# Optimization experiments

Hardware: AMD Instinct MI355X
Metric: run time of the kernel (lower is better)

## Reference

```python
import jax, jax.numpy as jnp
import numpy as np

B, S, D = 2, 2048, 2048
NH, NKV, HD = 16, 4, 128
ROPE_BASE = 10000.0
NEG = -1e9


def _rope_tables(seq_len, dim):
    inv_freq = 1.0 / ROPE_BASE ** (jnp.arange(0, dim, 2, dtype=jnp.float32) / dim)
    t = jnp.arange(seq_len, dtype=jnp.float32)
    freqs = jnp.outer(t, inv_freq)                      # [S, dim/2]
    return jnp.cos(freqs), jnp.sin(freqs)


def _apply_rope(x, cos, sin):
    # x: [B, S, H, HD]; interleaved-pair rotation matching the original module
    x1 = x[..., ::2]
    x2 = x[..., 1::2]
    c = cos[None, :, None, :]
    s = sin[None, :, None, :]
    out1 = x1 * c - x2 * s
    out2 = x1 * s + x2 * c
    return jnp.stack([out1, out2], axis=-1).reshape(x.shape)


def setup_inputs() -> dict:
    key = jax.random.key(0)
    ks = jax.random.split(key, 5)
    x = jax.random.normal(ks[0], (B, S, D), dtype=jnp.float32)
    # causal additive mask [1, 1, S, S]
    causal = jnp.tril(jnp.ones((S, S), dtype=jnp.bool_))
    mask = jnp.where(causal, 0.0, NEG).astype(jnp.float32)[None, None]
    Wq = jax.random.normal(ks[1], (D, NH * HD), dtype=jnp.float32) * (D ** -0.5)
    Wk = jax.random.normal(ks[2], (D, NKV * HD), dtype=jnp.float32) * (D ** -0.5)
    Wv = jax.random.normal(ks[3], (D, NKV * HD), dtype=jnp.float32) * (D ** -0.5)
    Wo = jax.random.normal(ks[4], (NH * HD, D), dtype=jnp.float32) * ((NH * HD) ** -0.5)
    return {"x": x, "mask": mask, "Wq": Wq, "Wk": Wk, "Wv": Wv, "Wo": Wo}


def reference(x, mask, Wq, Wk, Wv, Wo):
    b, s, _ = x.shape
    q = (x @ Wq).reshape(b, s, NH, HD)
    k = (x @ Wk).reshape(b, s, NKV, HD)
    v = (x @ Wv).reshape(b, s, NKV, HD)

    cos, sin = _rope_tables(s, HD)
    q = _apply_rope(q, cos, sin)
    k = _apply_rope(k, cos, sin)

    rep = NH // NKV
    k = jnp.repeat(k, rep, axis=2)                       # [b, s, NH, HD]
    v = jnp.repeat(v, rep, axis=2)

    q = q.transpose(0, 2, 1, 3)                          # [b, NH, s, HD]
    k = k.transpose(0, 2, 1, 3)
    v = v.transpose(0, 2, 1, 3)

    scores = jnp.einsum('bhqd,bhkd->bhqk', q, k) / jnp.sqrt(jnp.float32(HD))
    scores = scores + mask
    attn = jax.nn.softmax(scores, axis=-1)
    out = jnp.einsum('bhqk,bhkd->bhqd', attn, v)
    out = out.transpose(0, 2, 1, 3).reshape(b, s, NH * HD)
    return out @ Wo
```

## Files before the change

kernel.cpp:

```cpp
#include <hip/hip_runtime.h>
#include <stdint.h>

#define B_    2
#define S_    2048
#define D_    2048
#define NH_   16
#define NKV_  4
#define HD_   128
#define M_    (B_*S_)
#define NQKV_ 3072

typedef __bf16 bf16x8 __attribute__((ext_vector_type(8)));
typedef float  f32x4  __attribute__((ext_vector_type(4)));

__device__ __forceinline__ unsigned short f2bf(float f) {
    unsigned int u = __float_as_uint(f);
    u += 0x7fffu + ((u >> 16) & 1u);
    return (unsigned short)(u >> 16);
}

__device__ __forceinline__ unsigned short cvt_bf(float f) {
    __bf16 b = (__bf16)f;
    return *(unsigned short*)&b;
}

__device__ __forceinline__ void async_cp16(const unsigned short* g, unsigned short* l) {
    __builtin_amdgcn_global_load_lds((const __attribute__((address_space(1))) void*)g,
                                     (__attribute__((address_space(3))) void*)l, 16, 0, 0);
}

__global__ void prep(const float* __restrict__ x, unsigned short* __restrict__ xb,
                     const float* __restrict__ Wq, const float* __restrict__ Wk,
                     const float* __restrict__ Wv, const float* __restrict__ Wo,
                     unsigned short* __restrict__ Wqkvt, unsigned short* __restrict__ Wot,
                     float2* __restrict__ ctab) {
    __shared__ float tile[32][33];
    const int blk = blockIdx.x, tid = threadIdx.x;

    if (blk < 8192) {
        int idx = blk * 256 + tid;
        float4 v = ((const float4*)x)[idx];
        unsigned int lo = (unsigned int)f2bf(v.x) | ((unsigned int)f2bf(v.y) << 16);
        unsigned int hi = (unsigned int)f2bf(v.z) | ((unsigned int)f2bf(v.w) << 16);
        ((uint2*)xb)[idx] = make_uint2(lo, hi);
    } else if (blk < 18432) {
        const float* src; unsigned short* dst; int ncols, nx, bxy;
        if (blk < 12288)      { src = Wq; dst = Wqkvt;             ncols = 2048; nx = 64; bxy = blk - 8192; }
        else if (blk < 13312) { src = Wk; dst = Wqkvt + 2048*2048; ncols = 512;  nx = 16; bxy = blk - 12288; }
        else if (blk < 14336) { src = Wv; dst = Wqkvt + 2560*2048; ncols = 512;  nx = 16; bxy = blk - 13312; }
        else                  { src = Wo; dst = Wot;               ncols = 2048; nx = 64; bxy = blk - 14336; }
        int n0 = (bxy & (nx - 1)) * 32, k0 = (bxy / nx) * 32;
        int tx = tid & 31, ty = tid >> 5;
#pragma unroll
        for (int i = 0; i < 4; i++) {
            int k = k0 + ty + i * 8;
            tile[ty + i * 8][tx] = src[(long)k * ncols + n0 + tx];
        }
        __syncthreads();
#pragma unroll
        for (int i = 0; i < 4; i++) {
            int n = n0 + ty + i * 8;
            dst[(long)n * 2048 + k0 + tx] = f2bf(tile[tx][ty + i * 8]);
        }
    } else {
        int gid = (blk - 18432) * 256 + tid;
        int s = gid >> 6, i = gid & 63;
        float inv = exp2f(-(float)i * 0.20762050593046014f);
        float ang = (float)s * inv;
        float sn, cs; sincosf(ang, &sn, &cs);
        ctab[gid] = make_float2(cs, sn);
    }
}


__device__ __forceinline__ bf16x8 lds_frag(const unsigned short* hb, int r, int ks, int quad) {
    int p = (r * 128 + ks * 64 + quad * 16) ^ ((r & 4) << 3);
    return *(const bf16x8*)((const char*)hb + p);
}

__device__ __forceinline__ void stage_half(const unsigned short* g, int Kel,
                                           unsigned short* lhalf, int wid, int lane) {
#pragma unroll
    for (int i = 0; i < 2; i++) {
        int chunk = wid * 2 + i;
        int o = chunk * 1024 + lane * 16;
        int row = o >> 7;
        int cb = (o & 127) ^ ((row & 4) << 3);
        async_cp16((const unsigned short*)((const char*)g + (size_t)row * Kel * 2 + cb),
                   lhalf + chunk * 512);
    }
}

template<int MB, int NB>
__device__ __forceinline__ void cluster(f32x4 (*acc)[4], bf16x8 (*a)[2], bf16x8 (*b)[2]) {
    __builtin_amdgcn_sched_barrier(0);
    __builtin_amdgcn_s_barrier();
    asm volatile("s_waitcnt lgkmcnt(0)" ::: "memory");
    __builtin_amdgcn_sched_barrier(0);
    __builtin_amdgcn_s_setprio(1);
#pragma unroll
    for (int ks = 0; ks < 2; ks++)
#pragma unroll
        for (int mi = 0; mi < 4; mi++)
#pragma unroll
            for (int ni = 0; ni < 2; ni++)
                acc[MB + mi][NB + ni] = __builtin_amdgcn_mfma_f32_16x16x32_bf16(
                    a[mi][ks], b[ni][ks], acc[MB + mi][NB + ni], 0, 0, 0);
    __builtin_amdgcn_s_setprio(0);
    __builtin_amdgcn_sched_barrier(0);
    __builtin_amdgcn_s_barrier();
    __builtin_amdgcn_sched_barrier(0);
}

__device__ __forceinline__ void gemm256_core(const unsigned short* __restrict__ A,
                                             const unsigned short* __restrict__ Bt,
                                             const int K, const int m0, const int n0,
                                             char* sm, f32x4 (*acc)[4]) {
    const int tid  = threadIdx.x;
    const int lane = tid & 63, wid = tid >> 6;
    const int quad = lane >> 4, l16 = lane & 15;
    const int wm = wid >> 2, wn = wid & 3;

    unsigned short* sA00 = (unsigned short*)(sm);
    unsigned short* sA01 = (unsigned short*)(sm + 16384);
    unsigned short* sA10 = (unsigned short*)(sm + 32768);
    unsigned short* sA11 = (unsigned short*)(sm + 49152);
    unsigned short* sB00 = (unsigned short*)(sm + 65536);
    unsigned short* sB01 = (unsigned short*)(sm + 81920);
    unsigned short* sB10 = (unsigned short*)(sm + 98304);
    unsigned short* sB11 = (unsigned short*)(sm + 114688);

    const unsigned short* A0 = A  + (size_t)m0 * K;
    const unsigned short* A1 = A  + (size_t)(m0 + 128) * K;
    const unsigned short* B0 = Bt + (size_t)n0 * K;
    const unsigned short* B1 = Bt + (size_t)(n0 + 128) * K;

    stage_half(A0,      K, sA00, wid, lane);
    stage_half(B1,      K, sB01, wid, lane);
    stage_half(A1,      K, sA01, wid, lane);
    stage_half(B0,      K, sB00, wid, lane);
    __builtin_amdgcn_sched_barrier(0);
    stage_half(A0 + 64, K, sA10, wid, lane);
    stage_half(B1 + 64, K, sB11, wid, lane);
    stage_half(A1 + 64, K, sA11, wid, lane);
    asm volatile("s_waitcnt vmcnt(6)" ::: "memory");
    __builtin_amdgcn_sched_barrier(0);
    __builtin_amdgcn_s_barrier();
    __builtin_amdgcn_sched_barrier(0);

    const int NIT = K >> 7;
    for (int j = 0; j < NIT; ++j) {
        const bool st = (j < NIT - 1);
        const int kof1 = (2 * j + 1) * 64;
        const int kof2 = (2 * j + 2) * 64;
        const int kof3 = (2 * j + 3) * 64;
        bf16x8 af[4][2], bA[2][2], bB[2][2];

#pragma unroll
        for (int mi = 0; mi < 4; mi++)
#pragma unroll
            for (int ks = 0; ks < 2; ks++)
                af[mi][ks] = lds_frag(sA00, wm * 64 + mi * 16 + l16, ks, quad);
#pragma unroll
        for (int ni = 0; ni < 2; ni++)
#pragma unroll
            for (int ks = 0; ks < 2; ks++)
                bA[ni][ks] = lds_frag(sB00, wn * 32 + ni * 16 + l16, ks, quad);
        stage_half(B0 + kof1, K, sB10, wid, lane);
        cluster<0, 0>(acc, af, bA);

#pragma unroll
        for (int ni = 0; ni < 2; ni++)
#pragma unroll
            for (int ks = 0; ks < 2; ks++)
                bB[ni][ks] = lds_frag(sB01, wn * 32 + ni * 16 + l16, ks, quad);
        if (st) stage_half(A0 + kof2, K, sA00, wid, lane);
        cluster<0, 2>(acc, af, bB);

#pragma unroll
        for (int mi = 0; mi < 4; mi++)
#pragma unroll
            for (int ks = 0; ks < 2; ks++)
                af[mi][ks] = lds_frag(sA01, wm * 64 + mi * 16 + l16, ks, quad);
        if (st) stage_half(B1 + kof2, K, sB01, wid, lane);
        cluster<4, 2>(acc, af, bB);

#pragma unroll
        for (int ni = 0; ni < 2; ni++)
#pragma unroll
            for (int ks = 0; ks < 2; ks++)
                bA[ni][ks] = lds_frag(sB00, wn * 32 + ni * 16 + l16, ks, quad);
        if (st) {
            stage_half(A1 + kof2, K, sA01, wid, lane);
            asm volatile("s_waitcnt vmcnt(6)" ::: "memory");
        } else {
            asm volatile("s_waitcnt vmcnt(0)" ::: "memory");
        }
        cluster<4, 0>(acc, af, bA);

#pragma unroll
        for (int mi = 0; mi < 4; mi++)
#pragma unroll
            for (int ks = 0; ks < 2; ks++)
                af[mi][ks] = lds_frag(sA10, wm * 64 + mi * 16 + l16, ks, quad);
#pragma unroll
        for (int ni = 0; ni < 2; ni++)
#pragma unroll
            for (int ks = 0; ks < 2; ks++)
                bA[ni][ks] = lds_frag(sB10, wn * 32 + ni * 16 + l16, ks, quad);
        if (st) stage_half(B0 + kof2, K, sB00, wid, lane);
        cluster<0, 0>(acc, af, bA);

#pragma unroll
        for (int ni = 0; ni < 2; ni++)
#pragma unroll
            for (int ks = 0; ks < 2; ks++)
                bB[ni][ks] = lds_frag(sB11, wn * 32 + ni * 16 + l16, ks, quad);
        if (st) stage_half(A0 + kof3, K, sA10, wid, lane);
        cluster<0, 2>(acc, af, bB);

#pragma unroll
        for (int mi = 0; mi < 4; mi++)
#pragma unroll
            for (int ks = 0; ks < 2; ks++)
                af[mi][ks] = lds_frag(sA11, wm * 64 + mi * 16 + l16, ks, quad);
        if (st) stage_half(B1 + kof3, K, sB11, wid, lane);
        cluster<4, 2>(acc, af, bB);

#pragma unroll
        for (int ni = 0; ni < 2; ni++)
#pragma unroll
            for (int ks = 0; ks < 2; ks++)
                bA[ni][ks] = lds_frag(sB10, wn * 32 + ni * 16 + l16, ks, quad);
        if (st) {
            stage_half(A1 + kof3, K, sA11, wid, lane);
            asm volatile("s_waitcnt vmcnt(6)" ::: "memory");
        }
        cluster<4, 0>(acc, af, bA);
    }
}

__global__ __launch_bounds__(512, 2) void gemm_qkv256(const unsigned short* __restrict__ A,
                                                      const unsigned short* __restrict__ Bt,
                                                      const float2* __restrict__ ctab,
                                                      unsigned short* __restrict__ Qr,
                                                      unsigned short* __restrict__ Kr,
                                                      unsigned short* __restrict__ Vt) {
    extern __shared__ char sm[];
    const int m0 = blockIdx.y * 256, n0 = blockIdx.x * 256;
    f32x4 acc[8][4] = {};
    gemm256_core(A, Bt, D_, m0, n0, sm, acc);

    const int tid  = threadIdx.x;
    const int lane = tid & 63, wid = tid >> 6;
    const int quad = lane >> 4, l16 = lane & 15;
    const int wm = wid >> 2, wn = wid & 3;

    if (n0 < 2048) {
#pragma unroll
        for (int mt = 0; mt < 8; mt++) {
            int rowb = m0 + ((mt & 4) << 5) + wm * 64 + (mt & 3) * 16 + quad * 4;
#pragma unroll
            for (int nt = 0; nt < 4; nt++) {
                int col = n0 + ((nt & 2) << 6) + wn * 32 + (nt & 1) * 16 + l16;
                int h = col >> 7, d = col & 127;
#pragma unroll
                for (int r = 0; r < 4; r++) {
                    int row = rowb + r;
                    int s = row & 2047, b = row >> 11;
                    float2 cs = ctab[s * 64 + (d >> 1)];
                    float own = acc[mt][nt][r];
                    float other = __shfl_xor(own, 1);
                    float val = (d & 1) ? (other * cs.y + own * cs.x)
                                        : (own * cs.x - other * cs.y);
                    Qr[((size_t)(b * 16 + h) * 2048 + s) * 128 + d] = f2bf(val);
                }
            }
        }
    } else if (n0 < 2560) {
#pragma unroll
        for (int mt = 0; mt < 8; mt++) {
            int rowb = m0 + ((mt & 4) << 5) + wm * 64 + (mt & 3) * 16 + quad * 4;
#pragma unroll
            for (int nt = 0; nt < 4; nt++) {
                int col = n0 + ((nt & 2) << 6) + wn * 32 + (nt & 1) * 16 + l16;
                int kvh = (col - 2048) >> 7, d = col & 127;
#pragma unroll
                for (int r = 0; r < 4; r++) {
                    int row = rowb + r;
                    int s = row & 2047, b = row >> 11;
                    float2 cs = ctab[s * 64 + (d >> 1)];
                    float own = acc[mt][nt][r];
                    float other = __shfl_xor(own, 1);
                    float val = (d & 1) ? (other * cs.y + own * cs.x)
                                        : (own * cs.x - other * cs.y);
                    Kr[((size_t)(b * 4 + kvh) * 2048 + s) * 128 + d] = f2bf(val);
                }
            }
        }
    } else {
        unsigned short* tr = (unsigned short*)sm;
#pragma unroll
        for (int mt = 0; mt < 8; mt++) {
            int slb = ((mt & 4) << 5) + wm * 64 + (mt & 3) * 16 + quad * 4;
#pragma unroll
            for (int nt = 0; nt < 4; nt++) {
                int cl = ((nt & 2) << 6) + wn * 32 + (nt & 1) * 16 + l16;
#pragma unroll
                for (int r = 0; r < 4; r++)
                    tr[cl * 256 + ((slb + r) ^ ((cl & 7) << 3))] = f2bf(acc[mt][nt][r]);
            }
        }
        __syncthreads();
        const int bb = m0 >> 11, sbase = m0 & 2047;
#pragma unroll
        for (int pass = 0; pass < 16; pass++) {
            int idx = pass * 512 + tid;
            int cl = idx >> 5, sch = idx & 31;
            uint4 v = *(const uint4*)&tr[cl * 256 + ((sch * 8) ^ ((cl & 7) << 3))];
            int col = n0 + cl;
            int kvh = (col - 2560) >> 7, d = col & 127;
            *(uint4*)&Vt[((size_t)(bb * 4 + kvh) * 128 + d) * 2048 + sbase + sch * 8] = v;
        }
    }
}

__global__ __launch_bounds__(512, 2) void gemm_bt128x256(const unsigned short* __restrict__ A,
                                                         const unsigned short* __restrict__ Bt,
                                                         float* __restrict__ C) {
    extern __shared__ char sm[];
    const int K = NH_ * HD_;
    const int tid  = threadIdx.x;
    const int lane = tid & 63, wid = tid >> 6;
    const int quad = lane >> 4, l16 = lane & 15;
    const int wm = wid >> 2, wn = wid & 3;
    const int m0 = blockIdx.y * 128, n0 = blockIdx.x * 256;

    unsigned short* sA0  = (unsigned short*)(sm);
    unsigned short* sA1  = (unsigned short*)(sm + 16384);
    unsigned short* sB00 = (unsigned short*)(sm + 32768);
    unsigned short* sB01 = (unsigned short*)(sm + 49152);
    unsigned short* sB10 = (unsigned short*)(sm + 65536);
    unsigned short* sB11 = (unsigned short*)(sm + 81920);

    const unsigned short* A0 = A  + (size_t)m0 * K;
    const unsigned short* B0 = Bt + (size_t)n0 * K;
    const unsigned short* B1 = Bt + (size_t)(n0 + 128) * K;

    f32x4 acc[4][4] = {};

    stage_half(A0,      K, sA0,  wid, lane);
    stage_half(B0,      K, sB00, wid, lane);
    stage_half(B1,      K, sB01, wid, lane);
    __builtin_amdgcn_sched_barrier(0);
    stage_half(A0 + 64, K, sA1,  wid, lane);
    stage_half(B0 + 64, K, sB10, wid, lane);
    asm volatile("s_waitcnt vmcnt(6)" ::: "memory");
    __builtin_amdgcn_sched_barrier(0);
    __builtin_amdgcn_s_barrier();
    __builtin_amdgcn_sched_barrier(0);

    const int NIT = K >> 7;
    for (int j = 0; j < NIT; ++j) {
        const bool st = (j < NIT - 1);
        const int t1 = (2 * j + 1) * 64;
        const int t2 = (2 * j + 2) * 64;
        const int t3 = (2 * j + 3) * 64;
        bf16x8 af[4][2], bb[2][2];

#pragma unroll
        for (int mi = 0; mi < 4; mi++)
#pragma unroll
            for (int ks = 0; ks < 2; ks++)
                af[mi][ks] = lds_frag(sA0, wm * 64 + mi * 16 + l16, ks, quad);
#pragma unroll
        for (int ni = 0; ni < 2; ni++)
#pragma unroll
            for (int ks = 0; ks < 2; ks++)
                bb[ni][ks] = lds_frag(sB00, wn * 32 + ni * 16 + l16, ks, quad);
        stage_half(B1 + t1, K, sB11, wid, lane);
        asm volatile("s_waitcnt vmcnt(6)" ::: "memory");
        cluster<0, 0>(acc, af, bb);

#pragma unroll
        for (int ni = 0; ni < 2; ni++)
#pragma unroll
            for (int ks = 0; ks < 2; ks++)
                bb[ni][ks] = lds_frag(sB01, wn * 32 + ni * 16 + l16, ks, quad);
        if (st) {
            stage_half(A0 + t2, K, sA0,  wid, lane);
            stage_half(B0 + t2, K, sB00, wid, lane);
            asm volatile("s_waitcnt vmcnt(6)" ::: "memory");
        } else {
            asm volatile("s_waitcnt vmcnt(2)" ::: "memory");
        }
        cluster<0, 2>(acc, af, bb);

#pragma unroll
        for (int mi = 0; mi < 4; mi++)
#pragma unroll
            for (int ks = 0; ks < 2; ks++)
                af[mi][ks] = lds_frag(sA1, wm * 64 + mi * 16 + l16, ks, quad);
#pragma unroll
        for (int ni = 0; ni < 2; ni++)
#pragma unroll
            for (int ks = 0; ks < 2; ks++)
                bb[ni][ks] = lds_frag(sB10, wn * 32 + ni * 16 + l16, ks, quad);
        if (st) {
            stage_half(B1 + t2, K, sB01, wid, lane);
            asm volatile("s_waitcnt vmcnt(6)" ::: "memory");
        } else {
            asm volatile("s_waitcnt vmcnt(0)" ::: "memory");
        }
        cluster<0, 0>(acc, af, bb);

#pragma unroll
        for (int ni = 0; ni < 2; ni++)
#pragma unroll
            for (int ks = 0; ks < 2; ks++)
                bb[ni][ks] = lds_frag(sB11, wn * 32 + ni * 16 + l16, ks, quad);
        if (st) {
            stage_half(A0 + t3, K, sA1,  wid, lane);
            stage_half(B0 + t3, K, sB10, wid, lane);
            asm volatile("s_waitcnt vmcnt(6)" ::: "memory");
        }
        cluster<0, 2>(acc, af, bb);
    }

#pragma unroll
    for (int mi = 0; mi < 4; mi++) {
        int rowb = m0 + wm * 64 + mi * 16 + quad * 4;
#pragma unroll
        for (int nb = 0; nb < 2; nb++)
#pragma unroll
            for (int ni = 0; ni < 2; ni++) {
                int col = n0 + nb * 128 + wn * 32 + ni * 16 + l16;
#pragma unroll
                for (int r = 0; r < 4; r++)
                    C[(size_t)(rowb + r) * 2048 + col] = acc[mi][nb * 2 + ni][r];
            }
    }
}

__global__ __launch_bounds__(256) void attn_fwd(const unsigned short* __restrict__ Qr,
                                                const unsigned short* __restrict__ Kr,
                                                const unsigned short* __restrict__ Vt,
                                                unsigned short* __restrict__ O) {
    __shared__ char KsB[64 * 256];
    __shared__ char VsB[128 * 128];
    __shared__ unsigned short Ps[4][16][72];
    const int tid  = threadIdx.x;
    const int lane = tid & 63, wid = tid >> 6;
    const int quad = lane >> 4, l16 = lane & 15;
    const int pid = blockIdx.x, h = blockIdx.y, b = blockIdx.z;
    const int kvh = h >> 2;
    const unsigned short* qp = Qr + (long)(b * NH_ + h) * S_ * HD_;
    const char* kpB = (const char*)(Kr + (long)(b * NKV_ + kvh) * S_ * HD_);
    const char* vpB = (const char*)(Vt + (long)(b * NKV_ + kvh) * HD_ * S_);
    const float sc2 = 0.08838834764831845f * 1.4426950408889634f;

    const int wKb = (tid * 16) ^ ((((tid >> 4) & 7)) << 4);
    const int wVb = (tid * 16) ^ ((((tid >> 3) & 7)) << 4);
    const int gKb = tid * 16;
    const int gVb = (tid >> 3) * (S_ * 2) + (tid & 7) * 16;
    int kro[4], vro[2];
#pragma unroll
    for (int ks = 0; ks < 4; ks++)
        kro[ks] = l16 * 256 + ((ks * 64 + quad * 16) ^ ((l16 & 7) << 4));
#pragma unroll
    for (int ks2 = 0; ks2 < 2; ks2++)
        vro[ks2] = l16 * 128 + ((ks2 * 64 + quad * 16) ^ ((l16 & 7) << 4));

    bf16x8 ones;
#pragma unroll
    for (int i = 0; i < 8; i++) ones[i] = (__bf16)1.0f;

    for (int phase = 0; phase < 2; phase++) {
        const int qt = phase ? pid : 31 - pid;
        const int qw = qt * 64 + wid * 16;

        bf16x8 aq[4];
#pragma unroll
        for (int ks = 0; ks < 4; ks++)
            aq[ks] = *(const bf16x8*)&qp[(long)(qw + l16) * HD_ + ks * 32 + quad * 8];

        f32x4 o[8] = {};
        float mi[4], li[4];
#pragma unroll
        for (int r = 0; r < 4; r++) { mi[r] = -3.0e38f; li[r] = 0.f; }

        for (int kt = 0; kt <= qt; kt++) {
            const int kv0 = kt * 64;
            const char* kg = kpB + (size_t)kv0 * 256 + gKb;
            const char* vg = vpB + (size_t)kv0 * 2 + gVb;
            __syncthreads();
#pragma unroll
            for (int i = 0; i < 4; i++)
                *(uint4*)(KsB + wKb + i * 4096) = *(const uint4*)(kg + i * 4096);
#pragma unroll
            for (int i = 0; i < 4; i++)
                *(uint4*)(VsB + wVb + i * 4096) = *(const uint4*)(vg + (size_t)i * 32 * (S_ * 2));
            __syncthreads();

            f32x4 s[4] = {};
#pragma unroll
            for (int ks = 0; ks < 4; ks++)
#pragma unroll
                for (int nt = 0; nt < 4; nt++) {
                    bf16x8 kb = *(const bf16x8*)&KsB[kro[ks] + nt * 4096];
                    s[nt] = __builtin_amdgcn_mfma_f32_16x16x32_bf16(aq[ks], kb, s[nt], 0, 0, 0);
                }

            float mt4[4];
#pragma unroll
            for (int r = 0; r < 4; r++) mt4[r] = -3.0e38f;
            if (kv0 + 63 > qw) {
#pragma unroll
                for (int nt = 0; nt < 4; nt++) {
                    int kvp = kv0 + nt * 16 + l16;
#pragma unroll
                    for (int r = 0; r < 4; r++) {
                        float sv = s[nt][r] * sc2;
                        sv = (kvp <= qw + quad * 4 + r) ? sv : -1.0e30f;
                        s[nt][r] = sv;
                        mt4[r] = fmaxf(mt4[r], sv);
                    }
                }
            } else {
#pragma unroll
                for (int nt = 0; nt < 4; nt++)
#pragma unroll
                    for (int r = 0; r < 4; r++) {
                        float sv = s[nt][r] * sc2;
                        s[nt][r] = sv;
                        mt4[r] = fmaxf(mt4[r], sv);
                    }
            }
#pragma unroll
            for (int off = 1; off < 16; off <<= 1)
#pragma unroll
                for (int r = 0; r < 4; r++)
                    mt4[r] = fmaxf(mt4[r], __shfl_xor(mt4[r], off));

            bool grew = false;
#pragma unroll
            for (int r = 0; r < 4; r++) grew |= (mt4[r] > mi[r]);
            float al[4];
#pragma unroll
            for (int r = 0; r < 4; r++) {
                float mn = fmaxf(mi[r], mt4[r]);
                al[r] = exp2f(mi[r] - mn);
                mi[r] = mn;
            }
            if (__any(grew)) {
#pragma unroll
                for (int t = 0; t < 8; t++)
#pragma unroll
                    for (int r = 0; r < 4; r++) o[t][r] *= al[r];
            }
#pragma unroll
            for (int nt = 0; nt < 4; nt++)
#pragma unroll
                for (int r = 0; r < 4; r++)
                    s[nt][r] = exp2f(s[nt][r] - mi[r]);

#pragma unroll
            for (int nt = 0; nt < 4; nt++)
#pragma unroll
                for (int r = 0; r < 4; r++)
                    Ps[wid][quad * 4 + r][nt * 16 + l16] = cvt_bf(s[nt][r]);

            f32x4 sumf = {};
#pragma unroll
            for (int ks2 = 0; ks2 < 2; ks2++) {
                bf16x8 pa = *(const bf16x8*)&Ps[wid][l16][ks2 * 32 + quad * 8];
                sumf = __builtin_amdgcn_mfma_f32_16x16x32_bf16(pa, ones, sumf, 0, 0, 0);
#pragma unroll
                for (int vt = 0; vt < 8; vt++) {
                    bf16x8 vb = *(const bf16x8*)&VsB[vro[ks2] + vt * 2048];
                    o[vt] = __builtin_amdgcn_mfma_f32_16x16x32_bf16(pa, vb, o[vt], 0, 0, 0);
                }
            }
#pragma unroll
            for (int r = 0; r < 4; r++) li[r] = li[r] * al[r] + sumf[r];
        }

#pragma unroll
        for (int r = 0; r < 4; r++) {
            float inv_l = 1.0f / li[r];
            int qpos = qw + quad * 4 + r;
#pragma unroll
            for (int vt = 0; vt < 8; vt++) {
                float val = o[vt][r] * inv_l;
                O[(long)(b * S_ + qpos) * 2048 + h * 128 + vt * 16 + l16] = cvt_bf(val);
            }
        }
    }
}

extern "C" void kernel_launch(void* const* d_in, const int* in_sizes, int n_in,
                              void* d_out, int out_size, void* d_ws, size_t ws_size,
                              hipStream_t stream) {
    const float* x  = (const float*)d_in[0];
    const float* Wq = (const float*)d_in[2];
    const float* Wk = (const float*)d_in[3];
    const float* Wv = (const float*)d_in[4];
    const float* Wo = (const float*)d_in[5];

    char* ws = (char*)d_ws;
    unsigned short* xb    = (unsigned short*)(ws);
    unsigned short* Wqkvt = (unsigned short*)(ws + 16777216);
    unsigned short* Wot   = (unsigned short*)(ws + 29360128);
    float2*         ctab  = (float2*)        (ws + 37748736);
    unsigned short* Qr    = (unsigned short*)(ws + 38797312);
    unsigned short* Kr    = (unsigned short*)(ws + 55574528);
    unsigned short* Vt    = (unsigned short*)(ws + 63963136);
    unsigned short* attn  = (unsigned short*)(ws + 68157440);

    static int attr_set = 0;
    if (!attr_set) {
        hipFuncSetAttribute(reinterpret_cast<const void*>(gemm_qkv256),
                            hipFuncAttributeMaxDynamicSharedMemorySize, 131072);
        hipFuncSetAttribute(reinterpret_cast<const void*>(gemm_bt128x256),
                            hipFuncAttributeMaxDynamicSharedMemorySize, 98304);
        attr_set = 1;
    }

    prep<<<18944, 256, 0, stream>>>(x, xb, Wq, Wk, Wv, Wo, Wqkvt, Wot, ctab);

    gemm_qkv256<<<dim3(12, 16), 512, 131072, stream>>>(xb, Wqkvt, ctab, Qr, Kr, Vt);

    attn_fwd<<<dim3(16, NH_, B_), 256, 0, stream>>>(Qr, Kr, Vt, attn);

    gemm_bt128x256<<<dim3(8, 32), 512, 98304, stream>>>(attn, Wot, (float*)d_out);
}
```

Baseline: 332.8 us.

## Prefetch next K/V tile into registers during attention compute

```diff
diff --git a/kernel.cpp b/kernel.cpp
--- a/kernel.cpp
+++ b/kernel.cpp
@@ -442,10 +442,10 @@
     }
 }
 
-__global__ __launch_bounds__(256) void attn_fwd(const unsigned short* __restrict__ Qr,
-                                                const unsigned short* __restrict__ Kr,
-                                                const unsigned short* __restrict__ Vt,
-                                                unsigned short* __restrict__ O) {
+__global__ __launch_bounds__(256, 2) void attn_fwd(const unsigned short* __restrict__ Qr,
+                                                   const unsigned short* __restrict__ Kr,
+                                                   const unsigned short* __restrict__ Vt,
+                                                   unsigned short* __restrict__ O) {
     __shared__ char KsB[64 * 256];
     __shared__ char VsB[128 * 128];
     __shared__ unsigned short Ps[4][16][72];
@@ -489,19 +489,36 @@
 #pragma unroll
         for (int r = 0; r < 4; r++) { mi[r] = -3.0e38f; li[r] = 0.f; }
 
+        uint4 kv[4], vv[4];
+#pragma unroll
+        for (int i = 0; i < 4; i++) kv[i] = *(const uint4*)(kpB + gKb + i * 4096);
+#pragma unroll
+        for (int i = 0; i < 4; i++) vv[i] = *(const uint4*)(vpB + gVb + (size_t)i * 32 * (S_ * 2));
+
         for (int kt = 0; kt <= qt; kt++) {
+            __builtin_amdgcn_sched_barrier(0);
+            asm volatile("s_waitcnt vmcnt(0)" ::: "memory");
+            __builtin_amdgcn_s_barrier();
+            __builtin_amdgcn_sched_barrier(0);
+#pragma unroll
+            for (int i = 0; i < 4; i++) *(uint4*)(KsB + wKb + i * 4096) = kv[i];
+#pragma unroll
+            for (int i = 0; i < 4; i++) *(uint4*)(VsB + wVb + i * 4096) = vv[i];
+            {
+                const int kvn = (kt < qt ? kt + 1 : kt) * 64;
+                const char* kg = kpB + (size_t)kvn * 256 + gKb;
+                const char* vg = vpB + (size_t)kvn * 2 + gVb;
+#pragma unroll
+                for (int i = 0; i < 4; i++) kv[i] = *(const uint4*)(kg + i * 4096);
+#pragma unroll
+                for (int i = 0; i < 4; i++) vv[i] = *(const uint4*)(vg + (size_t)i * 32 * (S_ * 2));
+            }
+            __builtin_amdgcn_sched_barrier(0);
+            asm volatile("s_waitcnt lgkmcnt(0)" ::: "memory");
+            __builtin_amdgcn_s_barrier();
+            __builtin_amdgcn_sched_barrier(0);
+
             const int kv0 = kt * 64;
-            const char* kg = kpB + (size_t)kv0 * 256 + gKb;
-            const char* vg = vpB + (size_t)kv0 * 2 + gVb;
-            __syncthreads();
-#pragma unroll
-            for (int i = 0; i < 4; i++)
-                *(uint4*)(KsB + wKb + i * 4096) = *(const uint4*)(kg + i * 4096);
-#pragma unroll
-            for (int i = 0; i < 4; i++)
-                *(uint4*)(VsB + wVb + i * 4096) = *(const uint4*)(vg + (size_t)i * 32 * (S_ * 2));
-            __syncthreads();
-
             f32x4 s[4] = {};
 #pragma unroll
             for (int ks = 0; ks < 4; ks++)
```

Result: slower. 446.9 us (+34.3%).
